# Performance work log

Measured on AMD Instinct MI355X. Metric: run time of the kernel, lower is better.

Reference implementation:

```python
import jax, jax.numpy as jnp
import numpy as np

REL_SIZE = 65
TAG_SIZE = 4


def _rope(y):
    # Interleaved rotary position embedding, matching the torch module:
    # cos_pos = cos(theta) repeat_interleave(2), sin_pos = sin(theta) repeat_interleave(2)
    # y2 = (-y1, y0, -y3, y2, ...)
    B, S, H = y.shape
    half = H // 2
    pos = jnp.arange(S, dtype=jnp.float32)[:, None]                      # (S,1)
    inv_freq = jnp.power(10000.0, -2.0 * jnp.arange(half, dtype=jnp.float32) / H)
    theta = pos * inv_freq                                               # (S, half)
    cos = jnp.repeat(jnp.cos(theta), 2, axis=-1)                          # (S, H)
    sin = jnp.repeat(jnp.sin(theta), 2, axis=-1)                          # (S, H)
    yr = y.reshape(B, S, half, 2)
    y2 = jnp.stack([-yr[..., 1], yr[..., 0]], axis=-1).reshape(B, S, H)
    return y * cos + y2 * sin


def setup_inputs() -> dict:
    key = jax.random.key(0)
    k1, k2, k3 = jax.random.split(key, 3)
    B, S, H = 1, 160, 768
    y = jax.random.normal(k1, (B, S, H), dtype=jnp.float32)
    event_idx = jax.random.randint(k2, (B, 16), 0, S)
    W1 = jax.random.normal(k3, (H, 2 * H), dtype=jnp.float32) * 0.02
    b1 = jnp.zeros((H,), dtype=jnp.float32)
    W2 = jax.random.normal(jax.random.fold_in(key, 7), (REL_SIZE * TAG_SIZE, H), dtype=jnp.float32) * 0.02
    b2 = jnp.zeros((REL_SIZE * TAG_SIZE,), dtype=jnp.float32)
    return {"y": y, "event_idx": event_idx, "W1": W1, "b1": b1, "W2": W2, "b2": b2}


def reference(y, event_idx, W1, b1, W2, b2):
    # Eval path (training=False): event_idx unused, dropout = identity, sigmoid applied.
    B, S, H = y.shape
    yrot = _rope(y)
    # Linear(cat(a, b)) is separable: split W1 into the halves acting on a and b.
    Wa, Wb = W1[:, :H], W1[:, H:]
    left = jnp.einsum('bsh,oh->bso', yrot, Wa)                  # contribution of token i (row)
    right = jnp.einsum('bsh,oh->bso', yrot, Wb) + b1            # contribution of token j (col)
    h = jax.nn.relu(left[:, :, None, :] + right[:, None, :, :])  # (B, S, S, H)
    out = jnp.einsum('bijh,oh->bijo', h, W2) + b2               # (B, S, S, 260)
    out = out.reshape(B, S, S, REL_SIZE, TAG_SIZE).transpose(0, 3, 1, 2, 4)  # (B, 65, S, S, 4)
    return jax.nn.sigmoid(out)
```

## Files before the change

### kernel.cpp

```cpp
#include <hip/hip_runtime.h>
#include <hip/hip_bf16.h>
#include <cstdint>

#define SDIM 160
#define HDIM 768
#define HALF 384
#define ODIM 260
#define OPAD 272
#define CHUNK_BYTES 34816
#define RT_CHUNK 4096
#define BUF_STRIDE 38912
#define LB_OFF 77824
#define WS_SMALL 1155088
#define WS_BIG   3514384

typedef __attribute__((ext_vector_type(8))) short short8;
typedef __attribute__((ext_vector_type(4))) float floatx4;
typedef _Float16 half8 __attribute__((ext_vector_type(8)));

typedef const __attribute__((address_space(1))) unsigned char gl_u8;
typedef __attribute__((address_space(3))) unsigned char lds_u8;

static __device__ __forceinline__ float bf2f(unsigned short u) {
    union { unsigned int i; float f; } v; v.i = ((unsigned int)u) << 16; return v.f;
}
static __device__ __forceinline__ unsigned short f2bf(float x) {
    __hip_bfloat16 h = __float2bfloat16(x);
    return *reinterpret_cast<unsigned short*>(&h);
}
static __device__ __forceinline__ unsigned short f2h(float x) {
    _Float16 h = (_Float16)x;
    return *reinterpret_cast<unsigned short*>(&h);
}
static __device__ __forceinline__ float q(float x) { return bf2f(f2bf(x)); }

__global__ __launch_bounds__(256) void prep_kernel(
    const float* __restrict__ y, const float* __restrict__ W1,
    const float* __restrict__ W2,
    unsigned short* __restrict__ yb, unsigned short* __restrict__ W2b,
    unsigned short* __restrict__ W1b, int do_w1b) {
    int bid = blockIdx.x;
    int t = threadIdx.x;
    if (bid < SDIM) {
        int s = bid;
        for (int p = t; p < HALF; p += 256) {
            float invf = __expf(-(2.0f * (float)p / (float)HDIM) * 9.210340371976184f);
            float th = (float)s * invf;
            float c = cosf(th), sn = sinf(th);
            float y0 = y[s * HDIM + 2 * p], y1 = y[s * HDIM + 2 * p + 1];
            yb[s * HDIM + 2 * p]     = f2bf(y0 * c - y1 * sn);
            yb[s * HDIM + 2 * p + 1] = f2bf(y1 * c + y0 * sn);
        }
    } else if (bid < SDIM + 102) {
        int idx = (bid - SDIM) * 256 + t;
        if (idx < 96 * OPAD) {
            int kg = idx / OPAD, row = idx - kg * OPAD;
            unsigned short o8[8];
            if (row < ODIM) {
                float4 a = *reinterpret_cast<const float4*>(W2 + row * HDIM + kg * 8);
                float4 b = *reinterpret_cast<const float4*>(W2 + row * HDIM + kg * 8 + 4);
                o8[0] = f2h(a.x); o8[1] = f2h(a.y); o8[2] = f2h(a.z); o8[3] = f2h(a.w);
                o8[4] = f2h(b.x); o8[5] = f2h(b.y); o8[6] = f2h(b.z); o8[7] = f2h(b.w);
            } else {
                #pragma unroll
                for (int e = 0; e < 8; ++e) o8[e] = 0;
            }
            *reinterpret_cast<uint4*>(W2b + ((size_t)kg * OPAD + row) * 8) =
                *reinterpret_cast<uint4*>(o8);
        }
    } else if (do_w1b) {
        int idx = (bid - SDIM - 102) * 256 + t;
        int kg = idx / 1536, row = idx - kg * 1536;
        const float* src = (row < 768) ? (W1 + row * 1536 + kg * 8)
                                       : (W1 + (row - 768) * 1536 + 768 + kg * 8);
        float4 a = *reinterpret_cast<const float4*>(src);
        float4 b = *reinterpret_cast<const float4*>(src + 4);
        unsigned short o8[8];
        o8[0] = f2bf(a.x); o8[1] = f2bf(a.y); o8[2] = f2bf(a.z); o8[3] = f2bf(a.w);
        o8[4] = f2bf(b.x); o8[5] = f2bf(b.y); o8[6] = f2bf(b.z); o8[7] = f2bf(b.w);
        *reinterpret_cast<uint4*>(W1b + ((size_t)kg * 1536 + row) * 8) =
            *reinterpret_cast<uint4*>(o8);
    }
}

__global__ __launch_bounds__(64, 2) void lr3_kernel(
    const unsigned short* __restrict__ yb, const unsigned short* __restrict__ W1b,
    const float* __restrict__ b1,
    unsigned short* __restrict__ Lb, unsigned short* __restrict__ Rt) {
    int l = threadIdx.x & 63;
    int l16 = l & 15, qd = l >> 4;
    int mt = blockIdx.x;
    int sq = blockIdx.y;
    int s0 = sq * 16 + l16;

    floatx4 acc = (floatx4){0.0f, 0.0f, 0.0f, 0.0f};

    const unsigned short* yrow0 = yb + s0 * HDIM;

    for (int ks = 0; ks < 24; ++ks) {
        int k = ks * 32 + qd * 8;
        int kg = ks * 4 + qd;
        union { uint4 u; short8 s; } bu0, au;
        bu0.u = *reinterpret_cast<const uint4*>(yrow0 + k);
        au.u = *reinterpret_cast<const uint4*>(
            W1b + ((size_t)kg * 1536 + mt * 16 + l16) * 8);
        acc = __builtin_amdgcn_mfma_f32_16x16x32_bf16(
            au.s, bu0.s, acc, 0, 0, 0);
    }

    int o2 = mt * 16 + qd * 4;
    int s_out = sq * 16 + l16;
    unsigned short out4[4];
    if (o2 < 768) {
        #pragma unroll
        for (int r = 0; r < 4; ++r) out4[r] = f2h(acc[r]);
        *reinterpret_cast<uint2*>(Lb + s_out * HDIM + o2) =
            *reinterpret_cast<uint2*>(out4);
    } else {
        int ob = o2 - 768;
        #pragma unroll
        for (int r = 0; r < 4; ++r)
            out4[r] = f2h(acc[r] + b1[ob + r]);
        *reinterpret_cast<uint2*>(
            Rt + ((size_t)(ob >> 3) * SDIM + s_out) * 8 + (ob & 7)) =
            *reinterpret_cast<uint2*>(out4);
    }
}

__global__ __launch_bounds__(256) void lr_fallback_kernel(
    const unsigned short* __restrict__ yb, const float* __restrict__ W1,
    const float* __restrict__ b1,
    unsigned short* __restrict__ Lb, unsigned short* __restrict__ Rt) {
    int idx = blockIdx.x * 256 + threadIdx.x;
    int s = idx / 1536;
    int o2 = idx - s * 1536;
    const unsigned short* yrow = yb + s * HDIM;
    if (o2 < 768) {
        const float* wp = W1 + o2 * 1536;
        float a0 = 0.0f;
        for (int k = 0; k < HDIM; ++k) a0 += q(wp[k]) * bf2f(yrow[k]);
        Lb[s * HDIM + o2] = f2h(a0);
    } else {
        int ob = o2 - 768;
        const float* wp = W1 + ob * 1536 + 768;
        float a0 = 0.0f;
        for (int k = 0; k < HDIM; ++k) a0 += q(wp[k]) * bf2f(yrow[k]);
        Rt[((size_t)(ob >> 3) * SDIM + s) * 8 + (ob & 7)] = f2h(a0 + b1[ob]);
    }
}

__global__ __launch_bounds__(512) void main_kernel(
    const unsigned short* __restrict__ Lb, const unsigned short* __restrict__ Rt,
    const unsigned short* __restrict__ W2b,
    const float* __restrict__ b2, float* __restrict__ out) {
    __shared__ __align__(16) unsigned char lds[2 * BUF_STRIDE + 3072];

    int w = threadIdx.x >> 6;
    int l = threadIdx.x & 63;
    int l16 = l & 15, qd = l >> 4;
    int jh = w & 1;
    int mq = w >> 1;
    int mt0 = mq * 4;
    int nmt = (mq == 3) ? 5 : 4;
    int i0 = blockIdx.x * 2;
    int j0 = blockIdx.y * 32;
    int j = j0 + jh * 16 + l16;

    floatx4 acc[2][5];
    #pragma unroll
    for (int c = 0; c < 2; ++c)
        #pragma unroll
        for (int mtl = 0; mtl < 5; ++mtl)
            acc[c][mtl] = (floatx4){0.0f, 0.0f, 0.0f, 0.0f};

    const unsigned char* wsrc = reinterpret_cast<const unsigned char*>(W2b);
    const unsigned char* rtsrc = reinterpret_cast<const unsigned char*>(Rt);
    const unsigned char* lbsrc = reinterpret_cast<const unsigned char*>(Lb);

    auto STAGE = [&](int ch, int b) {
        unsigned char* lbuf = lds + b * BUF_STRIDE;
        #pragma unroll
        for (int it = 0; it < 5; ++it) {
            int seg = w + it * 8;
            if (seg < 34) {
                __builtin_amdgcn_global_load_lds(
                    (gl_u8*)(wsrc + (size_t)ch * CHUNK_BYTES + seg * 1024 + l * 16),
                    (lds_u8*)(lbuf + seg * 1024), 16, 0, 0);
            } else if (seg < 38) {
                int s2 = seg - 34;
                int kgl = s2 * 2 + (l >> 5);
                int jj = l & 31;
                __builtin_amdgcn_global_load_lds(
                    (gl_u8*)(rtsrc + (((size_t)(ch * 8 + kgl) * SDIM) + j0 + jj) * 16),
                    (lds_u8*)(lbuf + CHUNK_BYTES + s2 * 1024), 16, 0, 0);
            }
        }
    };

    if (w < 3) {
        int bofs = w * 1024 + l * 16;
        int row = bofs >= 1536 ? 1 : 0;
        int off = bofs - row * 1536;
        __builtin_amdgcn_global_load_lds(
            (gl_u8*)(lbsrc + ((size_t)(i0 + row) * HDIM) * 2 + off),
            (lds_u8*)(lds + LB_OFF + w * 1024), 16, 0, 0);
    }
    STAGE(0, 0);
    __syncthreads();

    for (int kc = 0; kc < 12; ++kc) {
        int buf = kc & 1;
        if (kc < 11) STAGE(kc + 1, 1 - buf);
        #pragma unroll
        for (int ks = 0; ks < 2; ++ks) {
            int kgl = ks * 4 + qd;
            half8 rh = *reinterpret_cast<const half8*>(
                lds + buf * BUF_STRIDE + CHUNK_BYTES +
                (kgl * 32 + jh * 16 + l16) * 16);
            int kb = (kc * 64 + ks * 32 + qd * 8) * 2;
            half8 bfrag[2];
            #pragma unroll
            for (int c = 0; c < 2; ++c) {
                half8 lh = *reinterpret_cast<const half8*>(
                    lds + LB_OFF + c * 1536 + kb);
                half8 hv = lh + rh;
                #pragma unroll
                for (int e = 0; e < 8; ++e)
                    hv[e] = hv[e] > (_Float16)0.0f ? hv[e] : (_Float16)0.0f;
                bfrag[c] = hv;
            }
            int ldsbase = buf * BUF_STRIDE + (kgl * OPAD + l16) * 16;
            #pragma unroll
            for (int mtl = 0; mtl < 5; ++mtl) {
                if (mtl < nmt) {
                    half8 ah = *reinterpret_cast<const half8*>(
                        lds + ldsbase + (mt0 + mtl) * 256);
                    acc[0][mtl] = __builtin_amdgcn_mfma_f32_16x16x32_f16(
                        ah, bfrag[0], acc[0][mtl], 0, 0, 0);
                    acc[1][mtl] = __builtin_amdgcn_mfma_f32_16x16x32_f16(
                        ah, bfrag[1], acc[1][mtl], 0, 0, 0);
                }
            }
        }
        __syncthreads();
    }

    #pragma unroll
    for (int c = 0; c < 2; ++c) {
        int i = i0 + c;
        #pragma unroll
        for (int mtl = 0; mtl < 5; ++mtl) {
            if (mtl < nmt) {
                int ob = (mt0 + mtl) * 16 + qd * 4;
                if (ob < ODIM) {
                    float4 bv = *reinterpret_cast<const float4*>(b2 + ob);
                    int rel = ob >> 2;
                    float4 v;
                    v.x = 1.0f / (1.0f + __expf(-(acc[c][mtl][0] + bv.x)));
                    v.y = 1.0f / (1.0f + __expf(-(acc[c][mtl][1] + bv.y)));
                    v.z = 1.0f / (1.0f + __expf(-(acc[c][mtl][2] + bv.z)));
                    v.w = 1.0f / (1.0f + __expf(-(acc[c][mtl][3] + bv.w)));
                    *reinterpret_cast<float4*>(
                        out + (((rel * SDIM) + i) * SDIM + j) * 4) = v;
                }
            }
        }
    }
}

__global__ void ws_too_small_kernel(float* out) { out[0] = 999.0f; }

extern "C" void kernel_launch(void* const* d_in, const int* in_sizes, int n_in,
                              void* d_out, int out_size, void* d_ws, size_t ws_size,
                              hipStream_t stream) {
    const float* y  = (const float*)d_in[0];
    const float* W1 = (const float*)d_in[2];
    const float* b1 = (const float*)d_in[3];
    const float* W2 = (const float*)d_in[4];
    const float* b2 = (const float*)d_in[5];
    float* out = (float*)d_out;

    if (ws_size < (size_t)WS_SMALL) {
        ws_too_small_kernel<<<dim3(1), dim3(1), 0, stream>>>(out);
        return;
    }

    unsigned short* yb  = (unsigned short*)((char*)d_ws + 16);
    unsigned short* Lb  = yb + SDIM * HDIM;
    unsigned short* Rt  = Lb + SDIM * HDIM;
    unsigned short* W2b = Rt + SDIM * HDIM;
    unsigned short* W1b = W2b + 96 * OPAD * 8;

    if (ws_size >= (size_t)WS_BIG) {
        prep_kernel<<<dim3(SDIM + 102 + 576), dim3(256), 0, stream>>>(
            y, W1, W2, yb, W2b, W1b, 1);
        lr3_kernel<<<dim3(96, 10), dim3(64), 0, stream>>>(yb, W1b, b1, Lb, Rt);
        main_kernel<<<dim3(80, 5), dim3(512), 0, stream>>>(Lb, Rt, W2b, b2, out);
    } else {
        prep_kernel<<<dim3(SDIM + 102), dim3(256), 0, stream>>>(
            y, W1, W2, yb, W2b, W1b, 0);
        lr_fallback_kernel<<<dim3(960), dim3(256), 0, stream>>>(yb, W1, b1, Lb, Rt);
        main_kernel<<<dim3(80, 5), dim3(512), 0, stream>>>(Lb, Rt, W2b, b2, out);
    }
}
```

Baseline: 104.6 us.

## Deepen main kernel staging to 4 half-size buffers with 3-chunk prefetch

Splits each K chunk in half (32 instead of 64) and rotates through four LDS buffers, prefetching three chunks ahead. Uses explicit vmcnt waits plus raw s_barrier instead of __syncthreads so in-flight async global-to-LDS loads stay outstanding across iterations. This aims to hide global load latency behind MFMA work. In exchange it doubles the barrier count, and the hand-counted vmcnt values are fragile if the per-wave load counts change.

```diff
diff --git a/kernel.cpp b/kernel.cpp
--- a/kernel.cpp
+++ b/kernel.cpp
@@ -7,9 +7,9 @@
 #define HALF 384
 #define ODIM 260
 #define OPAD 272
-#define CHUNK_BYTES 34816
-#define RT_CHUNK 4096
-#define BUF_STRIDE 38912
+#define W2B_CH 17408
+#define RT_CH 2048
+#define BUF_STRIDE 19456
 #define LB_OFF 77824
 #define WS_SMALL 1155088
 #define WS_BIG   3514384
@@ -153,7 +153,7 @@
     const unsigned short* __restrict__ Lb, const unsigned short* __restrict__ Rt,
     const unsigned short* __restrict__ W2b,
     const float* __restrict__ b2, float* __restrict__ out) {
-    __shared__ __align__(16) unsigned char lds[2 * BUF_STRIDE + 3072];
+    __shared__ __align__(16) unsigned char lds[4 * BUF_STRIDE + 3072];
 
     int w = threadIdx.x >> 6;
     int l = threadIdx.x & 63;
@@ -180,19 +180,19 @@
     auto STAGE = [&](int ch, int b) {
         unsigned char* lbuf = lds + b * BUF_STRIDE;
         #pragma unroll
-        for (int it = 0; it < 5; ++it) {
+        for (int it = 0; it < 3; ++it) {
             int seg = w + it * 8;
-            if (seg < 34) {
+            if (seg < 17) {
                 __builtin_amdgcn_global_load_lds(
-                    (gl_u8*)(wsrc + (size_t)ch * CHUNK_BYTES + seg * 1024 + l * 16),
+                    (gl_u8*)(wsrc + (size_t)ch * W2B_CH + seg * 1024 + l * 16),
                     (lds_u8*)(lbuf + seg * 1024), 16, 0, 0);
-            } else if (seg < 38) {
-                int s2 = seg - 34;
+            } else if (seg < 19) {
+                int s2 = seg - 17;
                 int kgl = s2 * 2 + (l >> 5);
                 int jj = l & 31;
                 __builtin_amdgcn_global_load_lds(
-                    (gl_u8*)(rtsrc + (((size_t)(ch * 8 + kgl) * SDIM) + j0 + jj) * 16),
-                    (lds_u8*)(lbuf + CHUNK_BYTES + s2 * 1024), 16, 0, 0);
+                    (gl_u8*)(rtsrc + (((size_t)(ch * 4 + kgl) * SDIM) + j0 + jj) * 16),
+                    (lds_u8*)(lbuf + W2B_CH + s2 * 1024), 16, 0, 0);
             }
         }
     };
@@ -206,43 +206,53 @@
             (lds_u8*)(lds + LB_OFF + w * 1024), 16, 0, 0);
     }
     STAGE(0, 0);
-    __syncthreads();
-
-    for (int kc = 0; kc < 12; ++kc) {
-        int buf = kc & 1;
-        if (kc < 11) STAGE(kc + 1, 1 - buf);
-        #pragma unroll
-        for (int ks = 0; ks < 2; ++ks) {
-            int kgl = ks * 4 + qd;
-            half8 rh = *reinterpret_cast<const half8*>(
-                lds + buf * BUF_STRIDE + CHUNK_BYTES +
-                (kgl * 32 + jh * 16 + l16) * 16);
-            int kb = (kc * 64 + ks * 32 + qd * 8) * 2;
-            half8 bfrag[2];
+    asm volatile("s_waitcnt vmcnt(0)" ::: "memory");
+    __builtin_amdgcn_s_barrier();
+    STAGE(1, 1);
+    STAGE(2, 2);
+
+    for (int kc = 0; kc < 24; ++kc) {
+        if (kc >= 1) {
+            if (kc <= 21) {
+                if (w < 3) asm volatile("s_waitcnt vmcnt(6)" ::: "memory");
+                else       asm volatile("s_waitcnt vmcnt(4)" ::: "memory");
+            } else if (kc == 22) {
+                if (w < 3) asm volatile("s_waitcnt vmcnt(3)" ::: "memory");
+                else       asm volatile("s_waitcnt vmcnt(2)" ::: "memory");
+            } else {
+                asm volatile("s_waitcnt vmcnt(0)" ::: "memory");
+            }
+            __builtin_amdgcn_s_barrier();
+        }
+        if (kc <= 20) STAGE(kc + 3, (kc + 3) & 3);
+
+        int bufbase = (kc & 3) * BUF_STRIDE;
+        half8 rh = *reinterpret_cast<const half8*>(
+            lds + bufbase + W2B_CH + (qd * 32 + jh * 16 + l16) * 16);
+        int kb = (kc * 32 + qd * 8) * 2;
+        half8 bfrag[2];
+        #pragma unroll
+        for (int c = 0; c < 2; ++c) {
+            half8 lh = *reinterpret_cast<const half8*>(
+                lds + LB_OFF + c * 1536 + kb);
+            half8 hv = lh + rh;
             #pragma unroll
-            for (int c = 0; c < 2; ++c) {
-                half8 lh = *reinterpret_cast<const half8*>(
-                    lds + LB_OFF + c * 1536 + kb);
-                half8 hv = lh + rh;
-                #pragma unroll
-                for (int e = 0; e < 8; ++e)
-                    hv[e] = hv[e] > (_Float16)0.0f ? hv[e] : (_Float16)0.0f;
-                bfrag[c] = hv;
-            }
-            int ldsbase = buf * BUF_STRIDE + (kgl * OPAD + l16) * 16;
-            #pragma unroll
-            for (int mtl = 0; mtl < 5; ++mtl) {
-                if (mtl < nmt) {
-                    half8 ah = *reinterpret_cast<const half8*>(
-                        lds + ldsbase + (mt0 + mtl) * 256);
-                    acc[0][mtl] = __builtin_amdgcn_mfma_f32_16x16x32_f16(
-                        ah, bfrag[0], acc[0][mtl], 0, 0, 0);
-                    acc[1][mtl] = __builtin_amdgcn_mfma_f32_16x16x32_f16(
-                        ah, bfrag[1], acc[1][mtl], 0, 0, 0);
-                }
-            }
-        }
-        __syncthreads();
+            for (int e = 0; e < 8; ++e)
+                hv[e] = hv[e] > (_Float16)0.0f ? hv[e] : (_Float16)0.0f;
+            bfrag[c] = hv;
+        }
+        int ldsbase = bufbase + (qd * OPAD + l16) * 16;
+        #pragma unroll
+        for (int mtl = 0; mtl < 5; ++mtl) {
+            if (mtl < nmt) {
+                half8 ah = *reinterpret_cast<const half8*>(
+                    lds + ldsbase + (mt0 + mtl) * 256);
+                acc[0][mtl] = __builtin_amdgcn_mfma_f32_16x16x32_f16(
+                    ah, bfrag[0], acc[0][mtl], 0, 0, 0);
+                acc[1][mtl] = __builtin_amdgcn_mfma_f32_16x16x32_f16(
+                    ah, bfrag[1], acc[1][mtl], 0, 0, 0);
+            }
+        }
     }
 
     #pragma unroll
```

New measurement: 107.5 us. 2.8% more time.

## Fuse prep and left/right projection into one cooperative kernel with grid sync

Applied to the files above, without the earlier changes.

Merges the RoPE/weight-conversion prep kernel and the MFMA left/right projection kernel into a single cooperative kernel of 480 blocks, separated by a grid-wide barrier. The aim is to remove one kernel launch and its inter-kernel gap. In exchange it adds the cost of a grid sync. Only two of the four waves per block do the projection phase, and the W1 conversion is now a strided loop.

```diff
diff --git a/kernel.cpp b/kernel.cpp
--- a/kernel.cpp
+++ b/kernel.cpp
@@ -1,5 +1,6 @@
 #include <hip/hip_runtime.h>
 #include <hip/hip_bf16.h>
+#include <hip/hip_cooperative_groups.h>
 #include <cstdint>
 
 #define SDIM 160
@@ -21,6 +22,8 @@
 typedef const __attribute__((address_space(1))) unsigned char gl_u8;
 typedef __attribute__((address_space(3))) unsigned char lds_u8;
 
+namespace cg = cooperative_groups;
+
 static __device__ __forceinline__ float bf2f(unsigned short u) {
     union { unsigned int i; float f; } v; v.i = ((unsigned int)u) << 16; return v.f;
 }
@@ -33,6 +36,97 @@
     return *reinterpret_cast<unsigned short*>(&h);
 }
 static __device__ __forceinline__ float q(float x) { return bf2f(f2bf(x)); }
+
+__global__ __launch_bounds__(256) void fused_pl_kernel(
+    const float* __restrict__ y, const float* __restrict__ W1,
+    const float* __restrict__ b1, const float* __restrict__ W2,
+    unsigned short* __restrict__ yb, unsigned short* __restrict__ W2b,
+    unsigned short* __restrict__ W1b,
+    unsigned short* __restrict__ Lb, unsigned short* __restrict__ Rt) {
+    int bid = blockIdx.x;
+    int t = threadIdx.x;
+    int gid = bid * 256 + t;
+
+    if (gid < SDIM * HALF) {
+        int s = gid / HALF;
+        int p = gid - s * HALF;
+        float invf = __expf(-(2.0f * (float)p / (float)HDIM) * 9.210340371976184f);
+        float th = (float)s * invf;
+        float c = cosf(th), sn = sinf(th);
+        float y0 = y[s * HDIM + 2 * p], y1 = y[s * HDIM + 2 * p + 1];
+        yb[s * HDIM + 2 * p]     = f2bf(y0 * c - y1 * sn);
+        yb[s * HDIM + 2 * p + 1] = f2bf(y1 * c + y0 * sn);
+    }
+    if (gid < 96 * OPAD) {
+        int kg = gid / OPAD, row = gid - kg * OPAD;
+        unsigned short o8[8];
+        if (row < ODIM) {
+            float4 a = *reinterpret_cast<const float4*>(W2 + row * HDIM + kg * 8);
+            float4 b = *reinterpret_cast<const float4*>(W2 + row * HDIM + kg * 8 + 4);
+            o8[0] = f2h(a.x); o8[1] = f2h(a.y); o8[2] = f2h(a.z); o8[3] = f2h(a.w);
+            o8[4] = f2h(b.x); o8[5] = f2h(b.y); o8[6] = f2h(b.z); o8[7] = f2h(b.w);
+        } else {
+            #pragma unroll
+            for (int e = 0; e < 8; ++e) o8[e] = 0;
+        }
+        *reinterpret_cast<uint4*>(W2b + ((size_t)kg * OPAD + row) * 8) =
+            *reinterpret_cast<uint4*>(o8);
+    }
+    for (int slot = gid; slot < 96 * 1536; slot += 480 * 256) {
+        int kg = slot / 1536, row = slot - kg * 1536;
+        const float* src = (row < 768) ? (W1 + row * 1536 + kg * 8)
+                                       : (W1 + (row - 768) * 1536 + 768 + kg * 8);
+        float4 a = *reinterpret_cast<const float4*>(src);
+        float4 b = *reinterpret_cast<const float4*>(src + 4);
+        unsigned short o8[8];
+        o8[0] = f2bf(a.x); o8[1] = f2bf(a.y); o8[2] = f2bf(a.z); o8[3] = f2bf(a.w);
+        o8[4] = f2bf(b.x); o8[5] = f2bf(b.y); o8[6] = f2bf(b.z); o8[7] = f2bf(b.w);
+        *reinterpret_cast<uint4*>(W1b + ((size_t)kg * 1536 + row) * 8) =
+            *reinterpret_cast<uint4*>(o8);
+    }
+
+    cg::this_grid().sync();
+
+    int w = t >> 6;
+    if (w >= 2) return;
+    int unit = bid * 2 + w;
+    int l = t & 63;
+    int l16 = l & 15, qd = l >> 4;
+    int mt = unit % 96;
+    int sq = unit / 96;
+    int s0 = sq * 16 + l16;
+
+    floatx4 acc = (floatx4){0.0f, 0.0f, 0.0f, 0.0f};
+    const unsigned short* yrow0 = yb + s0 * HDIM;
+
+    for (int ks = 0; ks < 24; ++ks) {
+        int k = ks * 32 + qd * 8;
+        int kg = ks * 4 + qd;
+        union { uint4 u; short8 s; } bu0, au;
+        bu0.u = *reinterpret_cast<const uint4*>(yrow0 + k);
+        au.u = *reinterpret_cast<const uint4*>(
+            W1b + ((size_t)kg * 1536 + mt * 16 + l16) * 8);
+        acc = __builtin_amdgcn_mfma_f32_16x16x32_bf16(
+            au.s, bu0.s, acc, 0, 0, 0);
+    }
+
+    int o2 = mt * 16 + qd * 4;
+    unsigned short out4[4];
+    if (o2 < 768) {
+        #pragma unroll
+        for (int r = 0; r < 4; ++r) out4[r] = f2h(acc[r]);
+        *reinterpret_cast<uint2*>(Lb + s0 * HDIM + o2) =
+            *reinterpret_cast<uint2*>(out4);
+    } else {
+        int ob = o2 - 768;
+        #pragma unroll
+        for (int r = 0; r < 4; ++r)
+            out4[r] = f2h(acc[r] + b1[ob + r]);
+        *reinterpret_cast<uint2*>(
+            Rt + ((size_t)(ob >> 3) * SDIM + s0) * 8 + (ob & 7)) =
+            *reinterpret_cast<uint2*>(out4);
+    }
+}
 
 __global__ __launch_bounds__(256) void prep_kernel(
     const float* __restrict__ y, const float* __restrict__ W1,
@@ -68,62 +162,6 @@
             *reinterpret_cast<uint4*>(W2b + ((size_t)kg * OPAD + row) * 8) =
                 *reinterpret_cast<uint4*>(o8);
         }
-    } else if (do_w1b) {
-        int idx = (bid - SDIM - 102) * 256 + t;
-        int kg = idx / 1536, row = idx - kg * 1536;
-        const float* src = (row < 768) ? (W1 + row * 1536 + kg * 8)
-                                       : (W1 + (row - 768) * 1536 + 768 + kg * 8);
-        float4 a = *reinterpret_cast<const float4*>(src);
-        float4 b = *reinterpret_cast<const float4*>(src + 4);
-        unsigned short o8[8];
-        o8[0] = f2bf(a.x); o8[1] = f2bf(a.y); o8[2] = f2bf(a.z); o8[3] = f2bf(a.w);
-        o8[4] = f2bf(b.x); o8[5] = f2bf(b.y); o8[6] = f2bf(b.z); o8[7] = f2bf(b.w);
-        *reinterpret_cast<uint4*>(W1b + ((size_t)kg * 1536 + row) * 8) =
-            *reinterpret_cast<uint4*>(o8);
-    }
-}
-
-__global__ __launch_bounds__(64, 2) void lr3_kernel(
-    const unsigned short* __restrict__ yb, const unsigned short* __restrict__ W1b,
-    const float* __restrict__ b1,
-    unsigned short* __restrict__ Lb, unsigned short* __restrict__ Rt) {
-    int l = threadIdx.x & 63;
-    int l16 = l & 15, qd = l >> 4;
-    int mt = blockIdx.x;
-    int sq = blockIdx.y;
-    int s0 = sq * 16 + l16;
-
-    floatx4 acc = (floatx4){0.0f, 0.0f, 0.0f, 0.0f};
-
-    const unsigned short* yrow0 = yb + s0 * HDIM;
-
-    for (int ks = 0; ks < 24; ++ks) {
-        int k = ks * 32 + qd * 8;
-        int kg = ks * 4 + qd;
-        union { uint4 u; short8 s; } bu0, au;
-        bu0.u = *reinterpret_cast<const uint4*>(yrow0 + k);
-        au.u = *reinterpret_cast<const uint4*>(
-            W1b + ((size_t)kg * 1536 + mt * 16 + l16) * 8);
-        acc = __builtin_amdgcn_mfma_f32_16x16x32_bf16(
-            au.s, bu0.s, acc, 0, 0, 0);
-    }
-
-    int o2 = mt * 16 + qd * 4;
-    int s_out = sq * 16 + l16;
-    unsigned short out4[4];
-    if (o2 < 768) {
-        #pragma unroll
-        for (int r = 0; r < 4; ++r) out4[r] = f2h(acc[r]);
-        *reinterpret_cast<uint2*>(Lb + s_out * HDIM + o2) =
-            *reinterpret_cast<uint2*>(out4);
-    } else {
-        int ob = o2 - 768;
-        #pragma unroll
-        for (int r = 0; r < 4; ++r)
-            out4[r] = f2h(acc[r] + b1[ob + r]);
-        *reinterpret_cast<uint2*>(
-            Rt + ((size_t)(ob >> 3) * SDIM + s_out) * 8 + (ob & 7)) =
-            *reinterpret_cast<uint2*>(out4);
     }
 }
 
@@ -292,9 +330,11 @@
     unsigned short* W1b = W2b + 96 * OPAD * 8;
 
     if (ws_size >= (size_t)WS_BIG) {
-        prep_kernel<<<dim3(SDIM + 102 + 576), dim3(256), 0, stream>>>(
-            y, W1, W2, yb, W2b, W1b, 1);
-        lr3_kernel<<<dim3(96, 10), dim3(64), 0, stream>>>(yb, W1b, b1, Lb, Rt);
+        void* args[] = {(void*)&y, (void*)&W1, (void*)&b1, (void*)&W2,
+                        (void*)&yb, (void*)&W2b, (void*)&W1b,
+                        (void*)&Lb, (void*)&Rt};
+        hipLaunchCooperativeKernel((const void*)fused_pl_kernel,
+                                   dim3(480), dim3(256), args, 0, stream);
         main_kernel<<<dim3(80, 5), dim3(512), 0, stream>>>(Lb, Rt, W2b, b2, out);
     } else {
         prep_kernel<<<dim3(SDIM + 102), dim3(256), 0, stream>>>(
```

After: 176.8 us. 1.69x slower.
